# Optimization experiments

Hardware: AMD Instinct MI355X
Metric: run time of the kernel (lower is better)

The kernel has to match this reference:

```python
import jax, jax.numpy as jnp
import numpy as np
from jax import lax

K = 3; KK = K * K; S = 1; P = 1; D = 1
BN_EPS = 1e-5


def setup_inputs() -> dict:
    key = jax.random.key(0)
    ks = jax.random.split(key, 4)
    B, C, H, W = 8, 128, 64, 64
    cout = 128
    # xavier-ish scales for conv weights
    def xavier(k, shape):
        fan_in = shape[1] * shape[2] * shape[3]
        fan_out = shape[0] * shape[2] * shape[3]
        limit = np.sqrt(6.0 / (fan_in + fan_out))
        return jax.random.uniform(k, shape, jnp.float32, -limit, limit)
    return {
        "x": jax.random.normal(ks[0], (B, C, H, W), jnp.float32),
        "w_off": xavier(ks[1], (2 * KK, C, K, K)),
        "b_off": jnp.zeros((2 * KK,), jnp.float32),
        "w_mod": xavier(ks[2], (KK, C, K, K)),
        "b_mod": jnp.zeros((KK,), jnp.float32),
        "w_reg": xavier(ks[3], (cout, C, K, K)),
        "b_reg": jnp.zeros((cout,), jnp.float32),
        "gamma": jnp.ones((cout,), jnp.float32),
        "beta": jnp.zeros((cout,), jnp.float32),
    }


def _conv(x, w, b):
    y = lax.conv_general_dilated(x, w, (S, S), [(P, P), (P, P)],
                                 rhs_dilation=(D, D),
                                 dimension_numbers=("NCHW", "OIHW", "NCHW"))
    return y + b[None, :, None, None]


def _deform_conv(x, offset, mask, w_reg, b_reg):
    B, C, H, W = x.shape
    Ho, Wo = offset.shape[2], offset.shape[3]
    # torchvision layout: [B, 2*KK, Ho, Wo], interleaved (dy, dx) per tap
    off = offset.reshape(B, KK, 2, Ho, Wo)
    dy, dx = off[:, :, 0], off[:, :, 1]                      # [B,KK,Ho,Wo]
    ki = jnp.arange(KK) // K
    kj = jnp.arange(KK) % K
    base_y = (jnp.arange(Ho) * S - P)[None, :, None] + (ki * D)[:, None, None]  # [KK,Ho,1]
    base_x = (jnp.arange(Wo) * S - P)[None, None, :] + (kj * D)[:, None, None]  # [KK,1,Wo]
    py = base_y[None].astype(x.dtype) + dy                   # [B,KK,Ho,Wo]
    px = base_x[None].astype(x.dtype) + dx

    y0f = jnp.floor(py); x0f = jnp.floor(px)
    ly = py - y0f; lx = px - x0f
    y0 = y0f.astype(jnp.int32); x0 = x0f.astype(jnp.int32)
    y1 = y0 + 1; x1 = x0 + 1

    def gather(iy, ix):
        valid = ((iy >= 0) & (iy < H) & (ix >= 0) & (ix < W)).astype(x.dtype)
        iyc = jnp.clip(iy, 0, H - 1)
        ixc = jnp.clip(ix, 0, W - 1)
        v = jax.vmap(lambda img, a, b: img[:, a, b])(x, iyc, ixc)  # [B,C,KK,Ho,Wo]
        return v * valid[:, None]

    val = (gather(y0, x0) * ((1 - ly) * (1 - lx))[:, None]
           + gather(y0, x1) * ((1 - ly) * lx)[:, None]
           + gather(y1, x0) * (ly * (1 - lx))[:, None]
           + gather(y1, x1) * (ly * lx)[:, None])               # [B,C,KK,Ho,Wo]

    patches = val * mask[:, None]                               # modulated samples
    wr = w_reg.reshape(w_reg.shape[0], C, KK)
    out = jnp.einsum("ock,bckhw->bohw", wr, patches)
    return out + b_reg[None, :, None, None]


def reference(x, w_off, b_off, w_mod, b_mod, w_reg, b_reg, gamma, beta):
    offset = _conv(x, w_off, b_off)
    modulator = 2.0 * jax.nn.sigmoid(_conv(x, w_mod, b_mod))
    y = _deform_conv(x, offset, modulator, w_reg, b_reg)
    # BatchNorm2d (training-mode batch statistics) + ReLU
    mu = y.mean(axis=(0, 2, 3), keepdims=True)
    var = y.var(axis=(0, 2, 3), keepdims=True)
    y = (y - mu) * lax.rsqrt(var + BN_EPS)
    y = y * gamma[None, :, None, None] + beta[None, :, None, None]
    return jax.nn.relu(y)
```

## Files before the change

### kernel.cpp

```cpp
#include <hip/hip_runtime.h>
#include <math.h>

#define H 64
#define W 64
#define C 128
#define NB 8
#define COUT 128
#define HWi 4096
#define NKC 36
#define PADu 40

typedef __attribute__((ext_vector_type(8))) short short8;
typedef __attribute__((ext_vector_type(8))) unsigned short ushort8;
typedef __attribute__((ext_vector_type(4))) unsigned short ushort4v;
typedef __attribute__((ext_vector_type(4))) float f32x4;

__device__ __forceinline__ unsigned short f2bf(float f){
    unsigned u = __float_as_uint(f);
    unsigned r = (u + 0x7FFFu + ((u >> 16) & 1u)) >> 16;
    return (unsigned short)r;
}
__device__ __forceinline__ float bf2f(unsigned short u){
    return __uint_as_float(((unsigned)u) << 16);
}

__global__ void k_pre(const float* __restrict__ x, unsigned short* __restrict__ xTp,
                      const float* __restrict__ w_reg, const float* __restrict__ w_off,
                      const float* __restrict__ w_mod, const float* __restrict__ b_off,
                      const float* __restrict__ b_mod,
                      unsigned short* __restrict__ wAv, unsigned short* __restrict__ w27A,
                      float* __restrict__ biasom, float* __restrict__ psum){
    int tid = threadIdx.x;
    if (blockIdx.x >= 528){
        int i = (blockIdx.x - 528) * 256 + tid;
        if (i < 147456){
            int kc = i >> 12, rem = i & 4095;
            int q = rem >> 10, r = (rem >> 3) & 127, j = rem & 7;
            int kk = kc * 32 + q * 8 + j, k = kk >> 7, c = kk & 127;
            wAv[i] = f2bf(w_reg[r * 1152 + c * 9 + k]);
        } else if (i < 147456 + 36864){
            int j2 = i - 147456;
            int kc = j2 >> 10, rem = j2 & 1023, m = rem >> 5, kkl = rem & 31;
            int kk = kc * 32 + kkl, k = kk >> 7, c = kk & 127;
            float v = 0.f;
            if (m < 18) v = w_off[m * 1152 + c * 9 + k];
            else if (m < 27) v = w_mod[(m - 18) * 1152 + c * 9 + k];
            w27A[j2] = f2bf(v);
        } else if (i < 147456 + 36864 + 32){
            int m = i - 147456 - 36864;
            biasom[m] = (m < 18) ? b_off[m] : (m < 27 ? b_mod[m - 18] : 0.f);
        } else if (i < 147456 + 36864 + 32 + 256){
            psum[i - 147456 - 36864 - 32] = 0.f;
        }
        return;
    }
    int bidx = blockIdx.x;
    int b = bidx & 7, hp = bidx >> 3;
    unsigned short* row = xTp + (size_t)(b * 66 + hp) * 66 * 128;
    if (hp == 0 || hp == 65){
        ushort8 z = {0,0,0,0,0,0,0,0};
        for (int i = tid; i < 66 * 128 / 8; i += 256) ((ushort8*)row)[i] = z;
        return;
    }
    int h = hp - 1;
    __shared__ unsigned short s[64 * 136];
    int w = tid & 63, c0 = tid >> 6;
    for (int cc = 0; cc < 128; cc += 4){
        int c = cc + c0;
        s[w * 136 + c] = f2bf(x[(size_t)(b * 128 + c) * HWi + h * 64 + w]);
    }
    __syncthreads();
    if (tid < 32){
        ushort8 z = {0,0,0,0,0,0,0,0};
        int wp = (tid < 16) ? 0 : 65;
        int sg = tid & 15;
        *(ushort8*)(row + wp * 128 + sg * 8) = z;
    }
    for (int it = tid; it < 1024; it += 256){
        int w2 = it >> 4, sg = it & 15;
        *(ushort8*)(row + (w2 + 1) * 128 + sg * 8) = *(const ushort8*)(s + w2 * 136 + sg * 8);
    }
}

__global__ __launch_bounds__(512, 4) void k_fused(const unsigned short* __restrict__ xTp,
        const unsigned short* __restrict__ w27A, const float* __restrict__ biasom,
        const unsigned short* __restrict__ wAv, const float* __restrict__ b_reg,
        unsigned short* __restrict__ ybf, float* __restrict__ psum){
    __shared__ char smem[79872];
    int tid = threadIdx.x;
    int lb = (blockIdx.x & 7) * 64 + (blockIdx.x >> 3);
    int n0 = lb * 64;
    int b = n0 >> 12, h = (n0 >> 6) & 63;

    {
        int grp = tid >> 8, gt = tid & 255;
        unsigned short* pA = (unsigned short*)(smem + grp * 15360);
        unsigned short* pB = (unsigned short*)(smem + grp * 15360 + 5120);
        int wvg = gt >> 6, lane = gt & 63, quad = lane >> 4, l16 = lane & 15;
        int nl = gt >> 2, sg = gt & 3;
        f32x4 acc0 = {0.f,0.f,0.f,0.f}, acc1 = {0.f,0.f,0.f,0.f};
        ushort8 rA, rB;
        int kc0 = grp * 18;
        auto p1load = [&](int i){
            int kc = kc0 + i;
            int k = kc >> 2, cb = (kc & 3) << 5;
            int ki = k / 3, kj = k - ki * 3;
            if (gt < 128) rA = *(const ushort8*)(w27A + kc * 1024 + gt * 8);
            int rowi = (b * 66 + h + ki) * 66 + (nl + kj);
            rB = *(const ushort8*)(xTp + (size_t)rowi * 128 + cb + sg * 8);
        };
        p1load(0);
        for (int i = 0; i < 18; i++){
            int p = i & 1;
            if (gt < 128) *(ushort8*)(pA + p * 1280 + (gt >> 2) * PADu + (gt & 3) * 8) = rA;
            *(ushort8*)(pB + p * 2560 + nl * PADu + sg * 8) = rB;
            if (i + 1 < 18) p1load(i + 1);
            __syncthreads();
            short8 bfrag = *(const short8*)(pB + p * 2560 + (wvg * 16 + l16) * PADu + quad * 8);
            short8 a0 = *(const short8*)(pA + p * 1280 + l16 * PADu + quad * 8);
            short8 a1 = *(const short8*)(pA + p * 1280 + (16 + l16) * PADu + quad * 8);
            acc0 = __builtin_amdgcn_mfma_f32_16x16x32_bf16(a0, bfrag, acc0, 0, 0, 0);
            acc1 = __builtin_amdgcn_mfma_f32_16x16x32_bf16(a1, bfrag, acc1, 0, 0, 0);
        }
        float* s_red = (float*)(smem + 30720);
        int npx = wvg * 16 + l16;
        if (grp == 1){
            #pragma unroll
            for (int t = 0; t < 2; t++){
                f32x4 a = t ? acc1 : acc0;
                #pragma unroll
                for (int r = 0; r < 4; r++)
                    s_red[npx * 32 + t * 16 + quad * 4 + r] = a[r];
            }
        }
        __syncthreads();
        if (grp == 0){
            unsigned short* s_OM = (unsigned short*)smem;
            #pragma unroll
            for (int t = 0; t < 2; t++){
                f32x4 a = t ? acc1 : acc0;
                #pragma unroll
                for (int r = 0; r < 4; r++){
                    int oc = t * 16 + quad * 4 + r;
                    float v = a[r] + s_red[npx * 32 + oc] + biasom[oc];
                    if (oc >= 18) v = 2.f / (1.f + expf(-v));
                    s_OM[npx * 32 + oc] = f2bf(v);
                }
            }
        }
        __syncthreads();
    }

    unsigned short* sA = (unsigned short*)smem;
    unsigned short* sB = (unsigned short*)(smem + 40960);
    int*   s_a0 = (int*)(smem + 61440);
    float* s_w0 = (float*)(smem + 70656);
    const unsigned short* s_OM = (const unsigned short*)smem;

    for (int idx = tid; idx < 576; idx += 512){
        int k = idx >> 6, px = idx & 63;
        float dy = bf2f(s_OM[px * 32 + 2 * k]);
        float dx = bf2f(s_OM[px * 32 + 2 * k + 1]);
        float m  = bf2f(s_OM[px * 32 + 18 + k]);
        int ki = k / 3, kj = k - ki * 3;
        float py  = (float)(h - 1 + ki) + dy;
        float pxf = (float)(px - 1 + kj) + dx;
        float y0f = floorf(py), x0f = floorf(pxf);
        float ly = py - y0f, lx = pxf - x0f;
        int iy0 = (int)y0f, ix0 = (int)x0f;
        int cy0 = min(max(iy0 + 1, 0), 65), cy1 = min(max(iy0 + 2, 0), 65);
        int cx0 = min(max(ix0 + 1, 0), 65), cx1 = min(max(ix0 + 2, 0), 65);
        int rb = b * 66 * 66;
        s_a0[0 * 576 + idx] = ((rb + cy0 * 66) + cx0) * 128;
        s_a0[1 * 576 + idx] = ((rb + cy0 * 66) + cx1) * 128;
        s_a0[2 * 576 + idx] = ((rb + cy1 * 66) + cx0) * 128;
        s_a0[3 * 576 + idx] = ((rb + cy1 * 66) + cx1) * 128;
        s_w0[0 * 576 + idx] = (1.f - ly) * (1.f - lx) * m;
        s_w0[1 * 576 + idx] = (1.f - ly) * lx * m;
        s_w0[2 * 576 + idx] = ly * (1.f - lx) * m;
        s_w0[3 * 576 + idx] = ly * lx * m;
    }
    __syncthreads();

    int wv = tid >> 6, lane = tid & 63, quad = lane >> 4, l16 = lane & 15;
    int ocq = wv & 3, ng = wv >> 2;
    int rA = tid & 127, qA = tid >> 7;
    int px = tid >> 3, cg = tid & 7;

    f32x4 acc00 = {0.f,0.f,0.f,0.f}, acc01 = {0.f,0.f,0.f,0.f};
    f32x4 acc10 = {0.f,0.f,0.f,0.f}, acc11 = {0.f,0.f,0.f,0.f};

    ushort8 rW0, rW1, rc0, rc1, rc2, rc3;
    float w0 = 0.f, w1 = 0.f, w2 = 0.f, w3 = 0.f;

    auto loadNextP = [&](int j){
        rW0 = *(const ushort8*)(wAv + (size_t)(2 * j) * 4096 + tid * 8);
        rW1 = *(const ushort8*)(wAv + (size_t)(2 * j + 1) * 4096 + tid * 8);
        int k = j >> 1, cb = (j & 1) << 6;
        int idx = k * 64 + px;
        int co = cb + cg * 8;
        w0 = s_w0[0 * 576 + idx]; w1 = s_w0[1 * 576 + idx];
        w2 = s_w0[2 * 576 + idx]; w3 = s_w0[3 * 576 + idx];
        rc0 = *(const ushort8*)(xTp + s_a0[0 * 576 + idx] + co);
        rc1 = *(const ushort8*)(xTp + s_a0[1 * 576 + idx] + co);
        rc2 = *(const ushort8*)(xTp + s_a0[2 * 576 + idx] + co);
        rc3 = *(const ushort8*)(xTp + s_a0[3 * 576 + idx] + co);
    };
    loadNextP(0);
    for (int j = 0; j < 18; j++){
        int p = j & 1;
        unsigned short* sAp = sA + p * 10240;
        unsigned short* sBp = sB + p * 5120;
        *(ushort8*)(sAp + rA * PADu + qA * 8) = rW0;
        *(ushort8*)(sAp + 5120 + rA * PADu + qA * 8) = rW1;
        {
            ushort8 o;
            #pragma unroll
            for (int s = 0; s < 8; s++){
                float v = w0 * bf2f(rc0[s]) + w1 * bf2f(rc1[s])
                        + w2 * bf2f(rc2[s]) + w3 * bf2f(rc3[s]);
                o[s] = f2bf(v);
            }
            *(ushort8*)(sBp + (cg >> 2) * 2560 + px * PADu + (cg & 3) * 8) = o;
        }
        if (j + 1 < 18) loadNextP(j + 1);
        __syncthreads();
        #pragma unroll
        for (int u = 0; u < 2; u++){
            const unsigned short* A = sAp + u * 5120;
            const unsigned short* Bn = sBp + u * 2560;
            short8 a0 = *(const short8*)(A + (ocq * 32 + l16) * PADu + quad * 8);
            short8 a1 = *(const short8*)(A + (ocq * 32 + 16 + l16) * PADu + quad * 8);
            short8 b0 = *(const short8*)(Bn + (ng * 32 + l16) * PADu + quad * 8);
            short8 b1 = *(const short8*)(Bn + (ng * 32 + 16 + l16) * PADu + quad * 8);
            acc00 = __builtin_amdgcn_mfma_f32_16x16x32_bf16(a0, b0, acc00, 0, 0, 0);
            acc01 = __builtin_amdgcn_mfma_f32_16x16x32_bf16(a0, b1, acc01, 0, 0, 0);
            acc10 = __builtin_amdgcn_mfma_f32_16x16x32_bf16(a1, b0, acc10, 0, 0, 0);
            acc11 = __builtin_amdgcn_mfma_f32_16x16x32_bf16(a1, b1, acc11, 0, 0, 0);
        }
    }

    __syncthreads();
    float* ls = (float*)smem;
    int sp0 = h * 64;
    #pragma unroll
    for (int to = 0; to < 2; to++){
        #pragma unroll
        for (int tn = 0; tn < 2; tn++){
            f32x4 a = to ? (tn ? acc11 : acc10) : (tn ? acc01 : acc00);
            int nl = ng * 32 + tn * 16 + l16;
            #pragma unroll
            for (int r = 0; r < 4; r++){
                int oc = ocq * 32 + to * 16 + quad * 4 + r;
                float v = a[r] + b_reg[oc];
                ybf[(size_t)(b * 128 + oc) * HWi + sp0 + nl] = f2bf(v);
                ls[oc * 68 + nl] = v;
            }
        }
    }
    __syncthreads();
    if (tid < 128){
        int oc = tid;
        float s = 0.f, s2 = 0.f;
        #pragma unroll 8
        for (int nl = 0; nl < 64; nl++){
            float v = ls[oc * 68 + nl];
            s += v; s2 = fmaf(v, v, s2);
        }
        atomicAdd(&psum[oc], s);
        atomicAdd(&psum[128 + oc], s2);
    }
}

__global__ void k_apply(const unsigned short* __restrict__ ybf, const float* __restrict__ psum,
                        const float* __restrict__ gamma, const float* __restrict__ beta,
                        float* __restrict__ out){
    int lb = ((int)blockIdx.x & 7) * 256 + ((int)blockIdx.x >> 3);
    int e8 = (lb * 256 + (int)threadIdx.x) * 8;
    int c = (e8 >> 12) & 127;
    ushort8 u = *(const ushort8*)(ybf + e8);
    float s = psum[c], s2 = psum[128 + c];
    float mean = s * (1.f / 32768.f);
    float var  = s2 * (1.f / 32768.f) - mean * mean;
    float rs = rsqrtf(var + 1e-5f);
    float g = gamma[c] * rs;
    float bt = beta[c] - mean * g;
    float4 lo, hi;
    lo.x = fmaxf(fmaf(bf2f(u[0]), g, bt), 0.f);
    lo.y = fmaxf(fmaf(bf2f(u[1]), g, bt), 0.f);
    lo.z = fmaxf(fmaf(bf2f(u[2]), g, bt), 0.f);
    lo.w = fmaxf(fmaf(bf2f(u[3]), g, bt), 0.f);
    hi.x = fmaxf(fmaf(bf2f(u[4]), g, bt), 0.f);
    hi.y = fmaxf(fmaf(bf2f(u[5]), g, bt), 0.f);
    hi.z = fmaxf(fmaf(bf2f(u[6]), g, bt), 0.f);
    hi.w = fmaxf(fmaf(bf2f(u[7]), g, bt), 0.f);
    *(float4*)(out + e8)     = lo;
    *(float4*)(out + e8 + 4) = hi;
}

extern "C" void kernel_launch(void* const* d_in, const int* in_sizes, int n_in,
                              void* d_out, int out_size, void* d_ws, size_t ws_size,
                              hipStream_t stream){
    const float* x     = (const float*)d_in[0];
    const float* w_off = (const float*)d_in[1];
    const float* b_off = (const float*)d_in[2];
    const float* w_mod = (const float*)d_in[3];
    const float* b_mod = (const float*)d_in[4];
    const float* w_reg = (const float*)d_in[5];
    const float* b_reg = (const float*)d_in[6];
    const float* gamma = (const float*)d_in[7];
    const float* beta  = (const float*)d_in[8];

    char* wsb = (char*)d_ws;
    unsigned short* xTp   = (unsigned short*)(wsb);
    unsigned short* ybf   = (unsigned short*)(wsb + 11018240);
    unsigned short* wAv   = (unsigned short*)(wsb + 19406848);
    unsigned short* w27A  = (unsigned short*)(wsb + 19701760);
    float*          biasom= (float*)(wsb + 19775488);
    float*          psum  = (float*)(wsb + 19775616);
    float* out = (float*)d_out;

    hipLaunchKernelGGL(k_pre,   dim3(1250), dim3(256), 0, stream, x, xTp, w_reg, w_off, w_mod, b_off, b_mod, wAv, w27A, biasom, psum);
    hipLaunchKernelGGL(k_fused, dim3(512),  dim3(512), 0, stream, xTp, w27A, biasom, wAv, b_reg, ybf, psum);
    hipLaunchKernelGGL(k_apply, dim3(2048), dim3(256), 0, stream, ybf, psum, gamma, beta, out);
}
```

Before: 134.1 us.

## Deepen register prefetch to two stages and swizzle LDS weight tiles

Both the offset/modulator conv loop and the main deformable GEMM loop now prefetch two iterations ahead using two alternating register sets, so global gathers have more time in flight before they are needed. The weight tile stores and reads in LDS use an XOR swizzle on the column chunk to reduce bank conflicts, and the per-channel stats scratch stride changes from 68 to 67 for the same reason. The deeper prefetch roughly doubles the live prefetch registers, which may cut occupancy under launch bounds of 512 threads and 4 blocks.

```diff
diff --git a/kernel.cpp b/kernel.cpp
--- a/kernel.cpp
+++ b/kernel.cpp
@@ -99,28 +99,33 @@
         int wvg = gt >> 6, lane = gt & 63, quad = lane >> 4, l16 = lane & 15;
         int nl = gt >> 2, sg = gt & 3;
         f32x4 acc0 = {0.f,0.f,0.f,0.f}, acc1 = {0.f,0.f,0.f,0.f};
-        ushort8 rA, rB;
         int kc0 = grp * 18;
-        auto p1load = [&](int i){
+        auto p1load = [&](int i, ushort8& A8, ushort8& B8){
             int kc = kc0 + i;
             int k = kc >> 2, cb = (kc & 3) << 5;
             int ki = k / 3, kj = k - ki * 3;
-            if (gt < 128) rA = *(const ushort8*)(w27A + kc * 1024 + gt * 8);
+            if (gt < 128) A8 = *(const ushort8*)(w27A + kc * 1024 + gt * 8);
             int rowi = (b * 66 + h + ki) * 66 + (nl + kj);
-            rB = *(const ushort8*)(xTp + (size_t)rowi * 128 + cb + sg * 8);
+            B8 = *(const ushort8*)(xTp + (size_t)rowi * 128 + cb + sg * 8);
         };
-        p1load(0);
-        for (int i = 0; i < 18; i++){
+        auto p1body = [&](int i, ushort8& A8, ushort8& B8){
             int p = i & 1;
-            if (gt < 128) *(ushort8*)(pA + p * 1280 + (gt >> 2) * PADu + (gt & 3) * 8) = rA;
-            *(ushort8*)(pB + p * 2560 + nl * PADu + sg * 8) = rB;
-            if (i + 1 < 18) p1load(i + 1);
+            if (gt < 128) *(ushort8*)(pA + p * 1280 + (gt >> 2) * PADu + (gt & 3) * 8) = A8;
+            *(ushort8*)(pB + p * 2560 + nl * PADu + sg * 8) = B8;
+            if (i + 2 < 18) p1load(i + 2, A8, B8);
             __syncthreads();
             short8 bfrag = *(const short8*)(pB + p * 2560 + (wvg * 16 + l16) * PADu + quad * 8);
             short8 a0 = *(const short8*)(pA + p * 1280 + l16 * PADu + quad * 8);
             short8 a1 = *(const short8*)(pA + p * 1280 + (16 + l16) * PADu + quad * 8);
             acc0 = __builtin_amdgcn_mfma_f32_16x16x32_bf16(a0, bfrag, acc0, 0, 0, 0);
             acc1 = __builtin_amdgcn_mfma_f32_16x16x32_bf16(a1, bfrag, acc1, 0, 0, 0);
+        };
+        ushort8 rA0, rB0, rA1, rB1;
+        p1load(0, rA0, rB0);
+        p1load(1, rA1, rB1);
+        for (int ih = 0; ih < 9; ih++){
+            p1body(ih * 2,     rA0, rB0);
+            p1body(ih * 2 + 1, rA1, rB1);
         }
         float* s_red = (float*)(smem + 30720);
         int npx = wvg * 16 + l16;
@@ -158,13 +163,13 @@
     const unsigned short* s_OM = (const unsigned short*)smem;
 
     for (int idx = tid; idx < 576; idx += 512){
-        int k = idx >> 6, px = idx & 63;
-        float dy = bf2f(s_OM[px * 32 + 2 * k]);
-        float dx = bf2f(s_OM[px * 32 + 2 * k + 1]);
-        float m  = bf2f(s_OM[px * 32 + 18 + k]);
+        int k = idx >> 6, px_ = idx & 63;
+        float dy = bf2f(s_OM[px_ * 32 + 2 * k]);
+        float dx = bf2f(s_OM[px_ * 32 + 2 * k + 1]);
+        float m  = bf2f(s_OM[px_ * 32 + 18 + k]);
         int ki = k / 3, kj = k - ki * 3;
         float py  = (float)(h - 1 + ki) + dy;
-        float pxf = (float)(px - 1 + kj) + dx;
+        float pxf = (float)(px_ - 1 + kj) + dx;
         float y0f = floorf(py), x0f = floorf(pxf);
         float ly = py - y0f, lx = pxf - x0f;
         int iy0 = (int)y0f, ix0 = (int)x0f;
@@ -185,59 +190,73 @@
     int wv = tid >> 6, lane = tid & 63, quad = lane >> 4, l16 = lane & 15;
     int ocq = wv & 3, ng = wv >> 2;
     int rA = tid & 127, qA = tid >> 7;
+    int cA = (qA ^ ((rA >> 3) & 3)) * 8;
     int px = tid >> 3, cg = tid & 7;
+
+    int rowA0 = ocq * 32 + l16, rowA1 = rowA0 + 16;
+    int offA0 = rowA0 * PADu + (quad ^ ((rowA0 >> 3) & 3)) * 8;
+    int offA1 = rowA1 * PADu + (quad ^ ((rowA1 >> 3) & 3)) * 8;
+    int offB0 = (ng * 32 + l16) * PADu + quad * 8;
+    int offB1 = (ng * 32 + 16 + l16) * PADu + quad * 8;
 
     f32x4 acc00 = {0.f,0.f,0.f,0.f}, acc01 = {0.f,0.f,0.f,0.f};
     f32x4 acc10 = {0.f,0.f,0.f,0.f}, acc11 = {0.f,0.f,0.f,0.f};
 
-    ushort8 rW0, rW1, rc0, rc1, rc2, rc3;
-    float w0 = 0.f, w1 = 0.f, w2 = 0.f, w3 = 0.f;
-
-    auto loadNextP = [&](int j){
-        rW0 = *(const ushort8*)(wAv + (size_t)(2 * j) * 4096 + tid * 8);
-        rW1 = *(const ushort8*)(wAv + (size_t)(2 * j + 1) * 4096 + tid * 8);
+    auto loadP = [&](int j, ushort8& W0, ushort8& W1, ushort8& C0, ushort8& C1,
+                     ushort8& C2, ushort8& C3, float4& Wt){
+        W0 = *(const ushort8*)(wAv + (size_t)(2 * j) * 4096 + tid * 8);
+        W1 = *(const ushort8*)(wAv + (size_t)(2 * j + 1) * 4096 + tid * 8);
         int k = j >> 1, cb = (j & 1) << 6;
         int idx = k * 64 + px;
         int co = cb + cg * 8;
-        w0 = s_w0[0 * 576 + idx]; w1 = s_w0[1 * 576 + idx];
-        w2 = s_w0[2 * 576 + idx]; w3 = s_w0[3 * 576 + idx];
-        rc0 = *(const ushort8*)(xTp + s_a0[0 * 576 + idx] + co);
-        rc1 = *(const ushort8*)(xTp + s_a0[1 * 576 + idx] + co);
-        rc2 = *(const ushort8*)(xTp + s_a0[2 * 576 + idx] + co);
-        rc3 = *(const ushort8*)(xTp + s_a0[3 * 576 + idx] + co);
+        Wt.x = s_w0[0 * 576 + idx]; Wt.y = s_w0[1 * 576 + idx];
+        Wt.z = s_w0[2 * 576 + idx]; Wt.w = s_w0[3 * 576 + idx];
+        C0 = *(const ushort8*)(xTp + s_a0[0 * 576 + idx] + co);
+        C1 = *(const ushort8*)(xTp + s_a0[1 * 576 + idx] + co);
+        C2 = *(const ushort8*)(xTp + s_a0[2 * 576 + idx] + co);
+        C3 = *(const ushort8*)(xTp + s_a0[3 * 576 + idx] + co);
     };
-    loadNextP(0);
-    for (int j = 0; j < 18; j++){
+    auto bodyP = [&](int j, ushort8& W0, ushort8& W1, ushort8& C0, ushort8& C1,
+                     ushort8& C2, ushort8& C3, float4& Wt){
         int p = j & 1;
         unsigned short* sAp = sA + p * 10240;
         unsigned short* sBp = sB + p * 5120;
-        *(ushort8*)(sAp + rA * PADu + qA * 8) = rW0;
-        *(ushort8*)(sAp + 5120 + rA * PADu + qA * 8) = rW1;
+        *(ushort8*)(sAp + rA * PADu + cA) = W0;
+        *(ushort8*)(sAp + 5120 + rA * PADu + cA) = W1;
         {
             ushort8 o;
             #pragma unroll
             for (int s = 0; s < 8; s++){
-                float v = w0 * bf2f(rc0[s]) + w1 * bf2f(rc1[s])
-                        + w2 * bf2f(rc2[s]) + w3 * bf2f(rc3[s]);
+                float v = Wt.x * bf2f(C0[s]) + Wt.y * bf2f(C1[s])
+                        + Wt.z * bf2f(C2[s]) + Wt.w * bf2f(C3[s]);
                 o[s] = f2bf(v);
             }
             *(ushort8*)(sBp + (cg >> 2) * 2560 + px * PADu + (cg & 3) * 8) = o;
         }
-        if (j + 1 < 18) loadNextP(j + 1);
+        if (j + 2 < 18) loadP(j + 2, W0, W1, C0, C1, C2, C3, Wt);
         __syncthreads();
         #pragma unroll
         for (int u = 0; u < 2; u++){
             const unsigned short* A = sAp + u * 5120;
             const unsigned short* Bn = sBp + u * 2560;
-            short8 a0 = *(const short8*)(A + (ocq * 32 + l16) * PADu + quad * 8);
-            short8 a1 = *(const short8*)(A + (ocq * 32 + 16 + l16) * PADu + quad * 8);
-            short8 b0 = *(const short8*)(Bn + (ng * 32 + l16) * PADu + quad * 8);
-            short8 b1 = *(const short8*)(Bn + (ng * 32 + 16 + l16) * PADu + quad * 8);
+            short8 a0 = *(const short8*)(A + offA0);
+            short8 a1 = *(const short8*)(A + offA1);
+            short8 b0 = *(const short8*)(Bn + offB0);
+            short8 b1 = *(const short8*)(Bn + offB1);
             acc00 = __builtin_amdgcn_mfma_f32_16x16x32_bf16(a0, b0, acc00, 0, 0, 0);
             acc01 = __builtin_amdgcn_mfma_f32_16x16x32_bf16(a0, b1, acc01, 0, 0, 0);
             acc10 = __builtin_amdgcn_mfma_f32_16x16x32_bf16(a1, b0, acc10, 0, 0, 0);
             acc11 = __builtin_amdgcn_mfma_f32_16x16x32_bf16(a1, b1, acc11, 0, 0, 0);
         }
+    };
+
+    ushort8 W0a, W1a, C0a, C1a, C2a, C3a, W0b, W1b, C0b, C1b, C2b, C3b;
+    float4 Wta, Wtb;
+    loadP(0, W0a, W1a, C0a, C1a, C2a, C3a, Wta);
+    loadP(1, W0b, W1b, C0b, C1b, C2b, C3b, Wtb);
+    for (int jh = 0; jh < 9; jh++){
+        bodyP(jh * 2,     W0a, W1a, C0a, C1a, C2a, C3a, Wta);
+        bodyP(jh * 2 + 1, W0b, W1b, C0b, C1b, C2b, C3b, Wtb);
     }
 
     __syncthreads();
@@ -254,7 +273,7 @@
                 int oc = ocq * 32 + to * 16 + quad * 4 + r;
                 float v = a[r] + b_reg[oc];
                 ybf[(size_t)(b * 128 + oc) * HWi + sp0 + nl] = f2bf(v);
-                ls[oc * 68 + nl] = v;
+                ls[oc * 67 + nl] = v;
             }
         }
     }
@@ -264,7 +283,7 @@
         float s = 0.f, s2 = 0.f;
         #pragma unroll 8
         for (int nl = 0; nl < 64; nl++){
-            float v = ls[oc * 68 + nl];
+            float v = ls[oc * 67 + nl];
             s += v; s2 = fmaf(v, v, s2);
         }
         atomicAdd(&psum[oc], s);
```

After: 132.4 us. Within noise of the previous version (-1.2%).
